# Performance work log

Hardware: AMD Instinct MI355X
Metric: run time of the kernel (lower is better)

Reference implementation:

```python
import jax, jax.numpy as jnp
import numpy as np

D_MODEL = 512
NUM_HEADS = 8
D_K = D_MODEL // NUM_HEADS
DIM_FF = 2048
EPS = 1e-5


def layer_norm(x, gamma, beta):
    mu = jnp.mean(x, axis=-1, keepdims=True)
    var = jnp.mean(jnp.square(x - mu), axis=-1, keepdims=True)
    return (x - mu) * jax.lax.rsqrt(var + EPS) * gamma + beta


def setup_inputs() -> dict:
    key = jax.random.key(0)
    ks = jax.random.split(key, 10)
    B, L = 8, 1024
    s = 1.0 / np.sqrt(D_MODEL)
    return {
        "h": jax.random.normal(ks[0], (B, L, D_MODEL), jnp.float32),
        "attn_bias": jax.random.normal(ks[1], (B, NUM_HEADS, L, L), jnp.float32),
        "mask": jnp.ones((B, L), jnp.int32),
        "Wqkv": jax.random.normal(ks[2], (D_MODEL, 3 * D_MODEL), jnp.float32) * s,
        "bqkv": jnp.zeros((3 * D_MODEL,), jnp.float32),
        "Wo": jax.random.normal(ks[3], (D_MODEL, D_MODEL), jnp.float32) * s,
        "bo": jnp.zeros((D_MODEL,), jnp.float32),
        "W1": jax.random.normal(ks[4], (D_MODEL, DIM_FF), jnp.float32) * s,
        "b1": jnp.zeros((DIM_FF,), jnp.float32),
        "W2": jax.random.normal(ks[5], (DIM_FF, D_MODEL), jnp.float32) * (1.0 / np.sqrt(DIM_FF)),
        "b2": jnp.zeros((D_MODEL,), jnp.float32),
        "g1": jnp.ones((D_MODEL,), jnp.float32),
        "be1": jnp.zeros((D_MODEL,), jnp.float32),
        "g2": jnp.ones((D_MODEL,), jnp.float32),
        "be2": jnp.zeros((D_MODEL,), jnp.float32),
    }


def reference(h, attn_bias, mask, Wqkv, bqkv, Wo, bo, W1, b1, W2, b2, g1, be1, g2, be2):
    B, L, D = h.shape
    H, dk = NUM_HEADS, D_K
    qkv = h @ Wqkv + bqkv                      # [B, L, 3D]
    q, k, v = jnp.split(qkv, 3, axis=-1)
    q = q.reshape(B, L, H, dk).transpose(0, 2, 1, 3)  # [B, H, L, dk]
    k = k.reshape(B, L, H, dk).transpose(0, 2, 1, 3)
    v = v.reshape(B, L, H, dk).transpose(0, 2, 1, 3)
    scores = jnp.einsum('bhqd,bhkd->bhqk', q, k) / np.sqrt(dk)
    scores = scores + attn_bias
    scores = jnp.where(mask[:, None, None, :] > 0, scores, -jnp.inf)
    attn = jax.nn.softmax(scores, axis=-1)
    out = jnp.einsum('bhqk,bhkd->bhqd', attn, v)       # [B, H, L, dk]
    out = out.transpose(0, 2, 1, 3).reshape(B, L, D)
    out = out @ Wo + bo
    h = layer_norm(h + out, g1, be1)
    ff = jax.nn.relu(h @ W1 + b1) @ W2 + b2
    h = layer_norm(h + ff, g2, be2)
    return h
```

## Files before the change

kernel.cpp:

```cpp
#include <hip/hip_runtime.h>
#include <hip/hip_bf16.h>
#include <math.h>

#define NUM_HEADS 8
#define SEQ_L 1024
#define EPS 1e-5f
#define KVBLK 64

typedef __bf16 bf16x8 __attribute__((ext_vector_type(8)));
typedef float f32x4 __attribute__((ext_vector_type(4)));
typedef __hip_bfloat16 bf16;

#define AS1 __attribute__((address_space(1)))
#define AS3 __attribute__((address_space(3)))

__device__ __forceinline__ void gload_lds16(const void* g, void* l) {
    __builtin_amdgcn_global_load_lds((const AS1 unsigned*)g, (AS3 unsigned*)l, 16, 0, 0);
}

__device__ __forceinline__ unsigned short bfb(float x) {
    bf16 b = __float2bfloat16(x);
    return *(unsigned short*)&b;
}

__device__ __forceinline__ int swz64(int el, int row) { return el ^ ((row & 7) << 3); }

__global__ __launch_bounds__(256) void f32_to_bf16_kernel(
    const float* __restrict__ in, bf16* __restrict__ out, int n)
{
    const int i = (blockIdx.x * 256 + threadIdx.x) * 4;
    if (i >= n) return;
    const float4 v = *(const float4*)&in[i];
    out[i + 0] = __float2bfloat16(v.x);
    out[i + 1] = __float2bfloat16(v.y);
    out[i + 2] = __float2bfloat16(v.z);
    out[i + 3] = __float2bfloat16(v.w);
}

__global__ __launch_bounds__(256) void transpose_w(
    const float* __restrict__ W, bf16* __restrict__ Wt, int K, int N)
{
    __shared__ float t[32][33];
    const int tx = threadIdx.x & 31, ty = threadIdx.x >> 5;
    const int n0 = blockIdx.x * 32, k0 = blockIdx.y * 32;
    #pragma unroll
    for (int r = 0; r < 4; ++r)
        t[ty + 8 * r][tx] = W[(size_t)(k0 + ty + 8 * r) * N + n0 + tx];
    __syncthreads();
    #pragma unroll
    for (int r = 0; r < 4; ++r)
        Wt[(size_t)(n0 + ty + 8 * r) * K + k0 + tx] = __float2bfloat16(t[tx][ty + 8 * r]);
}

__global__ __launch_bounds__(256) void gemm_bf16(
    const bf16* __restrict__ A, const bf16* __restrict__ Bt,
    const float* __restrict__ bias,
    float* __restrict__ C, bf16* __restrict__ Cb,
    int M, int N, int K, int relu)
{
    __shared__ __align__(16) bf16 Abuf[128 * 32];
    __shared__ __align__(16) bf16 Bbuf[128 * 32];
    const int tid = threadIdx.x;
    const int wv = tid >> 6, lane = tid & 63;
    const int row0 = blockIdx.y * 128, col0 = blockIdx.x * 128;
    const int wm = (wv >> 1) * 64, wn = (wv & 1) * 64;
    const int r0 = lane & 15, kb = lane >> 4;

    f32x4 acc[4][4] = {};
    const int arow = lane >> 2;
    const int akoff = (lane & 3) * 8;

    for (int k0 = 0; k0 < K; k0 += 32) {
        #pragma unroll
        for (int s = 0; s < 2; ++s) {
            const int c = 2 * wv + s;
            gload_lds16(&A[(size_t)(row0 + c * 16 + arow) * K + k0 + akoff], &Abuf[c * 512]);
            gload_lds16(&Bt[(size_t)(col0 + c * 16 + arow) * K + k0 + akoff], &Bbuf[c * 512]);
        }
        __syncthreads();

        bf16x8 a[4], b[4];
        #pragma unroll
        for (int i = 0; i < 4; ++i)
            a[i] = *(const bf16x8*)&Abuf[(wm + i * 16 + r0) * 32 + kb * 8];
        #pragma unroll
        for (int j = 0; j < 4; ++j)
            b[j] = *(const bf16x8*)&Bbuf[(wn + j * 16 + r0) * 32 + kb * 8];
        #pragma unroll
        for (int i = 0; i < 4; ++i)
            #pragma unroll
            for (int j = 0; j < 4; ++j)
                acc[i][j] = __builtin_amdgcn_mfma_f32_16x16x32_bf16(a[i], b[j], acc[i][j], 0, 0, 0);
        __syncthreads();
    }

    float bv[4];
    #pragma unroll
    for (int j = 0; j < 4; ++j) bv[j] = bias[col0 + wn + j * 16 + r0];

    #pragma unroll
    for (int i = 0; i < 4; ++i) {
        #pragma unroll
        for (int j = 0; j < 4; ++j) {
            const int col = col0 + wn + j * 16 + r0;
            #pragma unroll
            for (int reg = 0; reg < 4; ++reg) {
                const int row = row0 + wm + i * 16 + kb * 4 + reg;
                float v = acc[i][j][reg] + bv[j];
                if (relu) v = fmaxf(v, 0.f);
                if (C)  C[(size_t)row * N + col] = v;
                if (Cb) Cb[(size_t)row * N + col] = __float2bfloat16(v);
            }
        }
    }
}

__global__ __launch_bounds__(256) void gemm_qkv(
    const bf16* __restrict__ A, const bf16* __restrict__ Bt,
    const float* __restrict__ bias,
    bf16* __restrict__ Qb, bf16* __restrict__ Kb, bf16* __restrict__ Vtb,
    int M, int N, int K)
{
    __shared__ __align__(16) bf16 Abuf[128 * 32];
    __shared__ __align__(16) bf16 Bbuf[128 * 32];
    const int tid = threadIdx.x;
    const int wv = tid >> 6, lane = tid & 63;
    const int row0 = blockIdx.y * 128, col0 = blockIdx.x * 128;
    const int wm = (wv >> 1) * 64, wn = (wv & 1) * 64;
    const int r0 = lane & 15, kb = lane >> 4;

    f32x4 acc[4][4] = {};
    const int arow = lane >> 2;
    const int akoff = (lane & 3) * 8;

    for (int k0 = 0; k0 < K; k0 += 32) {
        #pragma unroll
        for (int s = 0; s < 2; ++s) {
            const int c = 2 * wv + s;
            gload_lds16(&A[(size_t)(row0 + c * 16 + arow) * K + k0 + akoff], &Abuf[c * 512]);
            gload_lds16(&Bt[(size_t)(col0 + c * 16 + arow) * K + k0 + akoff], &Bbuf[c * 512]);
        }
        __syncthreads();

        bf16x8 a[4], b[4];
        #pragma unroll
        for (int i = 0; i < 4; ++i)
            a[i] = *(const bf16x8*)&Abuf[(wm + i * 16 + r0) * 32 + kb * 8];
        #pragma unroll
        for (int j = 0; j < 4; ++j)
            b[j] = *(const bf16x8*)&Bbuf[(wn + j * 16 + r0) * 32 + kb * 8];
        #pragma unroll
        for (int i = 0; i < 4; ++i)
            #pragma unroll
            for (int j = 0; j < 4; ++j)
                acc[i][j] = __builtin_amdgcn_mfma_f32_16x16x32_bf16(a[i], b[j], acc[i][j], 0, 0, 0);
        __syncthreads();
    }

    #pragma unroll
    for (int i = 0; i < 4; ++i) {
        #pragma unroll
        for (int j = 0; j < 4; ++j) {
            const int col = col0 + wn + j * 16 + r0;
            const float bv = bias[col];
            const int region = col >> 9;
            const int cc = col & 511;
            const int head = cc >> 6, d = cc & 63;
            const int l0 = row0 + wm + i * 16 + kb * 4;
            const int b_ = l0 >> 10, l_ = l0 & 1023;
            if (region == 2) {
                unsigned short pk[4];
                #pragma unroll
                for (int reg = 0; reg < 4; ++reg) pk[reg] = bfb(acc[i][j][reg] + bv);
                *(ushort4*)&Vtb[((size_t)(b_ * NUM_HEADS + head) * 64 + d) * SEQ_L + l_] =
                    make_ushort4(pk[0], pk[1], pk[2], pk[3]);
            } else {
                const float s = (region == 0) ? 0.125f : 1.0f;
                bf16* dst = (region == 0) ? Qb : Kb;
                #pragma unroll
                for (int reg = 0; reg < 4; ++reg) {
                    dst[((size_t)(b_ * NUM_HEADS + head) * SEQ_L + l_ + reg) * 64 + d] =
                        __float2bfloat16((acc[i][j][reg] + bv) * s);
                }
            }
        }
    }
}

__global__ __launch_bounds__(256) void attn_mfma(
    const bf16* __restrict__ Qb, const bf16* __restrict__ Kb,
    const bf16* __restrict__ Vtb, const float* __restrict__ abias,
    const int* __restrict__ mask, bf16* __restrict__ out)
{
    const int bh = blockIdx.y;
    const int b = bh >> 3, h = bh & 7;
    const int q0 = blockIdx.x * 64;
    const int tid = threadIdx.x;
    const int wv = tid >> 6, lane = tid & 63;
    const int ql = lane & 15;
    const int hi = lane >> 4;

    __shared__ __align__(16) bf16 Ks[KVBLK * 64];
    __shared__ __align__(16) bf16 Vs[64 * KVBLK];
    __shared__ __align__(16) bf16 Ps[4][16 * 64];
    __shared__ float maskf[KVBLK];

    const int qrow = q0 + wv * 16 + ql;
    bf16x8 qf[2];
    #pragma unroll
    for (int kk = 0; kk < 2; ++kk)
        qf[kk] = *(const bf16x8*)&Qb[((size_t)bh * SEQ_L + qrow) * 64 + kk * 32 + hi * 8];

    f32x4 o[4] = {};
    float m = -1e30f, l = 0.f;

    const size_t bias_row = ((size_t)(b * NUM_HEADS + h) * SEQ_L + qrow) * SEQ_L;

    for (int k0 = 0; k0 < SEQ_L; k0 += KVBLK) {
        __syncthreads();
        {
            const int r = tid >> 3;
            const int c8 = (tid & 7) * 8;
            #pragma unroll
            for (int it = 0; it < 2; ++it) {
                const int row = r + it * 32;
                bf16x8 kv = *(const bf16x8*)&Kb[((size_t)bh * SEQ_L + k0 + row) * 64 + c8];
                *(bf16x8*)&Ks[swz64(row * 64 + c8, row)] = kv;
                bf16x8 vv = *(const bf16x8*)&Vtb[((size_t)bh * 64 + row) * SEQ_L + k0 + c8];
                *(bf16x8*)&Vs[swz64(row * 64 + c8, row)] = vv;
            }
            if (tid < KVBLK)
                maskf[tid] = (mask[b * SEQ_L + k0 + tid] > 0) ? 0.f : -1e30f;
        }
        __syncthreads();

        f32x4 bias4[4];
        #pragma unroll
        for (int c = 0; c < 4; ++c)
            bias4[c] = *(const f32x4*)&abias[bias_row + k0 + c * 16 + hi * 4];

        float p[4][4];
        #pragma unroll
        for (int c = 0; c < 4; ++c) {
            f32x4 sacc = {};
            #pragma unroll
            for (int kk = 0; kk < 2; ++kk) {
                const int row = c * 16 + ql;
                bf16x8 kf = *(const bf16x8*)&Ks[swz64(row * 64 + kk * 32 + hi * 8, row)];
                sacc = __builtin_amdgcn_mfma_f32_16x16x32_bf16(kf, qf[kk], sacc, 0, 0, 0);
            }
            const f32x4 mk = *(const f32x4*)&maskf[c * 16 + hi * 4];
            #pragma unroll
            for (int reg = 0; reg < 4; ++reg)
                p[c][reg] = sacc[reg] + bias4[c][reg] + mk[reg];
        }

        float mx = p[0][0];
        #pragma unroll
        for (int c = 0; c < 4; ++c)
            #pragma unroll
            for (int reg = 0; reg < 4; ++reg) mx = fmaxf(mx, p[c][reg]);
        mx = fmaxf(mx, __shfl_xor(mx, 16, 64));
        mx = fmaxf(mx, __shfl_xor(mx, 32, 64));

        const float mnew = fmaxf(m, mx);
        const float scale = __expf(m - mnew);
        m = mnew;
        float lsum = 0.f;
        #pragma unroll
        for (int c = 0; c < 4; ++c)
            #pragma unroll
            for (int reg = 0; reg < 4; ++reg) {
                const float pv = (p[c][reg] > -1e29f) ? __expf(p[c][reg] - mnew) : 0.f;
                p[c][reg] = pv;
                lsum += pv;
            }
        lsum += __shfl_xor(lsum, 16, 64);
        lsum += __shfl_xor(lsum, 32, 64);
        l = l * scale + lsum;

        #pragma unroll
        for (int c = 0; c < 4; ++c)
            #pragma unroll
            for (int s2 = 0; s2 < 2; ++s2) {
                const int el = ql * 64 + c * 16 + hi * 4 + 2 * s2;
                const unsigned pk = (unsigned)bfb(p[c][2 * s2]) |
                                    ((unsigned)bfb(p[c][2 * s2 + 1]) << 16);
                *(unsigned*)&Ps[wv][swz64(el, ql)] = pk;
            }

        #pragma unroll
        for (int reg = 0; reg < 4; ++reg) {
            const float sc_q = __shfl(scale, (lane & 48) | (hi * 4 + reg), 64);
            #pragma unroll
            for (int c2 = 0; c2 < 4; ++c2) o[c2][reg] *= sc_q;
        }

        #pragma unroll
        for (int kk = 0; kk < 2; ++kk) {
            bf16x8 pf = *(const bf16x8*)&Ps[wv][swz64(ql * 64 + kk * 32 + hi * 8, ql)];
            #pragma unroll
            for (int c2 = 0; c2 < 4; ++c2) {
                const int vrow = c2 * 16 + ql;
                bf16x8 vf = *(const bf16x8*)&Vs[swz64(vrow * 64 + kk * 32 + hi * 8, vrow)];
                o[c2] = __builtin_amdgcn_mfma_f32_16x16x32_bf16(pf, vf, o[c2], 0, 0, 0);
            }
        }
    }

    const float invl = (l > 0.f) ? (1.0f / l) : 0.f;
    #pragma unroll
    for (int reg = 0; reg < 4; ++reg) {
        const float inv_q = __shfl(invl, (lane & 48) | (hi * 4 + reg), 64);
        const int row = q0 + wv * 16 + hi * 4 + reg;
        #pragma unroll
        for (int c2 = 0; c2 < 4; ++c2)
            out[((size_t)(b * SEQ_L + row)) * 512 + h * 64 + c2 * 16 + ql] =
                __float2bfloat16(o[c2][reg] * inv_q);
    }
}

__global__ __launch_bounds__(256) void add_ln_kernel(
    const float* __restrict__ X, const float* __restrict__ Y,
    const float* __restrict__ gamma, const float* __restrict__ beta,
    float* __restrict__ out, bf16* __restrict__ outb)
{
    const int wave = threadIdx.x >> 6;
    const int lane = threadIdx.x & 63;
    const int row = blockIdx.x * 4 + wave;
    const float* xp = X + (size_t)row * 512 + lane * 8;
    const float* yp = Y + (size_t)row * 512 + lane * 8;

    float v[8];
    const float4 a0 = *(const float4*)xp;
    const float4 a1 = *(const float4*)(xp + 4);
    const float4 b0 = *(const float4*)yp;
    const float4 b1 = *(const float4*)(yp + 4);
    v[0] = a0.x + b0.x; v[1] = a0.y + b0.y; v[2] = a0.z + b0.z; v[3] = a0.w + b0.w;
    v[4] = a1.x + b1.x; v[5] = a1.y + b1.y; v[6] = a1.z + b1.z; v[7] = a1.w + b1.w;

    float s = 0.f, sq = 0.f;
    #pragma unroll
    for (int i = 0; i < 8; ++i) { s += v[i]; sq += v[i] * v[i]; }
    #pragma unroll
    for (int off = 1; off < 64; off <<= 1) {
        s += __shfl_xor(s, off, 64);
        sq += __shfl_xor(sq, off, 64);
    }
    const float mu = s * (1.f / 512.f);
    const float var = sq * (1.f / 512.f) - mu * mu;
    const float rstd = rsqrtf(var + EPS);

    const int c = lane * 8;
    const float4 g0 = *(const float4*)&gamma[c];
    const float4 g1 = *(const float4*)&gamma[c + 4];
    const float4 e0 = *(const float4*)&beta[c];
    const float4 e1 = *(const float4*)&beta[c + 4];
    float r[8];
    r[0] = (v[0] - mu) * rstd * g0.x + e0.x;
    r[1] = (v[1] - mu) * rstd * g0.y + e0.y;
    r[2] = (v[2] - mu) * rstd * g0.z + e0.z;
    r[3] = (v[3] - mu) * rstd * g0.w + e0.w;
    r[4] = (v[4] - mu) * rstd * g1.x + e1.x;
    r[5] = (v[5] - mu) * rstd * g1.y + e1.y;
    r[6] = (v[6] - mu) * rstd * g1.z + e1.z;
    r[7] = (v[7] - mu) * rstd * g1.w + e1.w;

    float* op = out + (size_t)row * 512 + c;
    *(float4*)op = make_float4(r[0], r[1], r[2], r[3]);
    *(float4*)(op + 4) = make_float4(r[4], r[5], r[6], r[7]);
    if (outb) {
        bf16* ob = outb + (size_t)row * 512 + c;
        #pragma unroll
        for (int i = 0; i < 8; ++i) ob[i] = __float2bfloat16(r[i]);
    }
}

extern "C" void kernel_launch(void* const* d_in, const int* in_sizes, int n_in,
                              void* d_out, int out_size, void* d_ws, size_t ws_size,
                              hipStream_t stream)
{
    const float* h    = (const float*)d_in[0];
    const float* ab   = (const float*)d_in[1];
    const int*   mask = (const int*)d_in[2];
    const float* Wqkv = (const float*)d_in[3];
    const float* bqkv = (const float*)d_in[4];
    const float* Wo   = (const float*)d_in[5];
    const float* bo   = (const float*)d_in[6];
    const float* W1   = (const float*)d_in[7];
    const float* b1   = (const float*)d_in[8];
    const float* W2   = (const float*)d_in[9];
    const float* b2   = (const float*)d_in[10];
    const float* g1   = (const float*)d_in[11];
    const float* be1  = (const float*)d_in[12];
    const float* g2   = (const float*)d_in[13];
    const float* be2  = (const float*)d_in[14];
    float* out = (float*)d_out;
    char* ws = (char*)d_ws;

    const int M = 8 * 1024;
    const size_t MB = 1024 * 1024;

    bf16*  hb   = (bf16*)(ws + 0 * MB);
    bf16*  Wtq  = (bf16*)(ws + 8 * MB);
    bf16*  Wto  = (bf16*)(ws + 10 * MB);
    bf16*  Wt1  = (bf16*)(ws + 11 * MB);
    bf16*  Wt2  = (bf16*)(ws + 13 * MB);
    bf16*  Qb   = (bf16*)(ws + 15 * MB);
    bf16*  Kb   = (bf16*)(ws + 23 * MB);
    bf16*  Vtb  = (bf16*)(ws + 31 * MB);
    bf16*  aob  = (bf16*)(ws + 39 * MB);
    float* proj = (float*)(ws + 47 * MB);
    float* h1   = (float*)(ws + 63 * MB);
    bf16*  h1b  = (bf16*)(ws + 79 * MB);
    bf16*  ffb  = (bf16*)(ws + 15 * MB);
    float* f2   = (float*)(ws + 47 * MB);

    f32_to_bf16_kernel<<<dim3(M * 512 / 1024), 256, 0, stream>>>(h, hb, M * 512);
    transpose_w<<<dim3(1536 / 32, 512 / 32), 256, 0, stream>>>(Wqkv, Wtq, 512, 1536);
    transpose_w<<<dim3(512 / 32, 512 / 32), 256, 0, stream>>>(Wo, Wto, 512, 512);
    transpose_w<<<dim3(2048 / 32, 512 / 32), 256, 0, stream>>>(W1, Wt1, 512, 2048);
    transpose_w<<<dim3(512 / 32, 2048 / 32), 256, 0, stream>>>(W2, Wt2, 2048, 512);

    gemm_qkv<<<dim3(1536 / 128, M / 128), 256, 0, stream>>>(hb, Wtq, bqkv, Qb, Kb, Vtb, M, 1536, 512);
    attn_mfma<<<dim3(SEQ_L / 64, 64), 256, 0, stream>>>(Qb, Kb, Vtb, ab, mask, aob);
    gemm_bf16<<<dim3(512 / 128, M / 128), 256, 0, stream>>>(aob, Wto, bo, proj, nullptr, M, 512, 512, 0);
    add_ln_kernel<<<dim3(M / 4), 256, 0, stream>>>(h, proj, g1, be1, h1, h1b);
    gemm_bf16<<<dim3(2048 / 128, M / 128), 256, 0, stream>>>(h1b, Wt1, b1, nullptr, ffb, M, 2048, 512, 1);
    gemm_bf16<<<dim3(512 / 128, M / 128), 256, 0, stream>>>(ffb, Wt2, b2, f2, nullptr, M, 512, 2048, 0);
    add_ln_kernel<<<dim3(M / 4), 256, 0, stream>>>(h1, f2, g2, be2, out, nullptr);
}
```

Before: 268.3 us.

## Double-buffer K/V tiles with register prefetch and use exp2 softmax in attention

```diff
diff --git a/kernel.cpp b/kernel.cpp
--- a/kernel.cpp
+++ b/kernel.cpp
@@ -6,6 +6,7 @@
 #define SEQ_L 1024
 #define EPS 1e-5f
 #define KVBLK 64
+#define LOG2E 1.44269504088896f
 
 typedef __bf16 bf16x8 __attribute__((ext_vector_type(8)));
 typedef float f32x4 __attribute__((ext_vector_type(4)));
@@ -175,7 +176,7 @@
                 *(ushort4*)&Vtb[((size_t)(b_ * NUM_HEADS + head) * 64 + d) * SEQ_L + l_] =
                     make_ushort4(pk[0], pk[1], pk[2], pk[3]);
             } else {
-                const float s = (region == 0) ? 0.125f : 1.0f;
+                const float s = (region == 0) ? (0.125f * LOG2E) : 1.0f;
                 bf16* dst = (region == 0) ? Qb : Kb;
                 #pragma unroll
                 for (int reg = 0; reg < 4; ++reg) {
@@ -200,10 +201,10 @@
     const int ql = lane & 15;
     const int hi = lane >> 4;
 
-    __shared__ __align__(16) bf16 Ks[KVBLK * 64];
-    __shared__ __align__(16) bf16 Vs[64 * KVBLK];
+    __shared__ __align__(16) bf16 Ks[2][KVBLK * 64];
+    __shared__ __align__(16) bf16 Vs[2][64 * KVBLK];
     __shared__ __align__(16) bf16 Ps[4][16 * 64];
-    __shared__ float maskf[KVBLK];
+    __shared__ float maskf[2][KVBLK];
 
     const int qrow = q0 + wv * 16 + ql;
     bf16x8 qf[2];
@@ -211,49 +212,73 @@
     for (int kk = 0; kk < 2; ++kk)
         qf[kk] = *(const bf16x8*)&Qb[((size_t)bh * SEQ_L + qrow) * 64 + kk * 32 + hi * 8];
 
+    const int sr = tid >> 3;
+    const int sc8 = (tid & 7) * 8;
+
     f32x4 o[4] = {};
     float m = -1e30f, l = 0.f;
-
     const size_t bias_row = ((size_t)(b * NUM_HEADS + h) * SEQ_L + qrow) * SEQ_L;
 
+    bf16x8 kreg[2], vreg[2];
+    f32x4 bias_raw[4];
+    float mreg = 0.f;
+    #pragma unroll
+    for (int it = 0; it < 2; ++it) {
+        const int row = sr + it * 32;
+        kreg[it] = *(const bf16x8*)&Kb[((size_t)bh * SEQ_L + row) * 64 + sc8];
+        vreg[it] = *(const bf16x8*)&Vtb[((size_t)bh * 64 + row) * SEQ_L + sc8];
+    }
+    #pragma unroll
+    for (int c = 0; c < 4; ++c)
+        bias_raw[c] = *(const f32x4*)&abias[bias_row + c * 16 + hi * 4];
+    if (tid < KVBLK) mreg = (mask[b * SEQ_L + tid] > 0) ? 0.f : -1e30f;
+    #pragma unroll
+    for (int it = 0; it < 2; ++it) {
+        const int row = sr + it * 32;
+        *(bf16x8*)&Ks[0][swz64(row * 64 + sc8, row)] = kreg[it];
+        *(bf16x8*)&Vs[0][swz64(row * 64 + sc8, row)] = vreg[it];
+    }
+    if (tid < KVBLK) maskf[0][tid] = mreg;
+
+    int cur = 0;
     for (int k0 = 0; k0 < SEQ_L; k0 += KVBLK) {
+        const bool more = (k0 + KVBLK) < SEQ_L;
+        f32x4 biasn[4];
+        if (more) {
+            const int k1 = k0 + KVBLK;
+            #pragma unroll
+            for (int it = 0; it < 2; ++it) {
+                const int row = sr + it * 32;
+                kreg[it] = *(const bf16x8*)&Kb[((size_t)bh * SEQ_L + k1 + row) * 64 + sc8];
+                vreg[it] = *(const bf16x8*)&Vtb[((size_t)bh * 64 + row) * SEQ_L + k1 + sc8];
+            }
+            #pragma unroll
+            for (int c = 0; c < 4; ++c)
+                biasn[c] = *(const f32x4*)&abias[bias_row + k1 + c * 16 + hi * 4];
+            if (tid < KVBLK) mreg = (mask[b * SEQ_L + k1 + tid] > 0) ? 0.f : -1e30f;
+        }
         __syncthreads();
-        {
-            const int r = tid >> 3;
-            const int c8 = (tid & 7) * 8;
-            #pragma unroll
-            for (int it = 0; it < 2; ++it) {
-                const int row = r + it * 32;
-                bf16x8 kv = *(const bf16x8*)&Kb[((size_t)bh * SEQ_L + k0 + row) * 64 + c8];
-                *(bf16x8*)&Ks[swz64(row * 64 + c8, row)] = kv;
-                bf16x8 vv = *(const bf16x8*)&Vtb[((size_t)bh * 64 + row) * SEQ_L + k0 + c8];
-                *(bf16x8*)&Vs[swz64(row * 64 + c8, row)] = vv;
-            }
-            if (tid < KVBLK)
-                maskf[tid] = (mask[b * SEQ_L + k0 + tid] > 0) ? 0.f : -1e30f;
-        }
-        __syncthreads();
-
-        f32x4 bias4[4];
-        #pragma unroll
-        for (int c = 0; c < 4; ++c)
-            bias4[c] = *(const f32x4*)&abias[bias_row + k0 + c * 16 + hi * 4];
-
-        float p[4][4];
+
+        f32x4 p[4];
         #pragma unroll
         for (int c = 0; c < 4; ++c) {
-            f32x4 sacc = {};
+            const f32x4 mk = *(const f32x4*)&maskf[cur][c * 16 + hi * 4];
+            #pragma unroll
+            for (int reg = 0; reg < 4; ++reg)
+                p[c][reg] = fmaf(bias_raw[c][reg], LOG2E, mk[reg]);
+        }
+
+        __builtin_amdgcn_s_setprio(1);
+        #pragma unroll
+        for (int c = 0; c < 4; ++c) {
+            const int row = c * 16 + ql;
             #pragma unroll
             for (int kk = 0; kk < 2; ++kk) {
-                const int row = c * 16 + ql;
-                bf16x8 kf = *(const bf16x8*)&Ks[swz64(row * 64 + kk * 32 + hi * 8, row)];
-                sacc = __builtin_amdgcn_mfma_f32_16x16x32_bf16(kf, qf[kk], sacc, 0, 0, 0);
-            }
-            const f32x4 mk = *(const f32x4*)&maskf[c * 16 + hi * 4];
-            #pragma unroll
-            for (int reg = 0; reg < 4; ++reg)
-                p[c][reg] = sacc[reg] + bias4[c][reg] + mk[reg];
-        }
+                bf16x8 kf = *(const bf16x8*)&Ks[cur][swz64(row * 64 + kk * 32 + hi * 8, row)];
+                p[c] = __builtin_amdgcn_mfma_f32_16x16x32_bf16(kf, qf[kk], p[c], 0, 0, 0);
+            }
+        }
+        __builtin_amdgcn_s_setprio(0);
 
         float mx = p[0][0];
         #pragma unroll
@@ -264,14 +289,14 @@
         mx = fmaxf(mx, __shfl_xor(mx, 32, 64));
 
         const float mnew = fmaxf(m, mx);
-        const float scale = __expf(m - mnew);
+        const float scale = __builtin_exp2f(m - mnew);
         m = mnew;
         float lsum = 0.f;
         #pragma unroll
         for (int c = 0; c < 4; ++c)
             #pragma unroll
             for (int reg = 0; reg < 4; ++reg) {
-                const float pv = (p[c][reg] > -1e29f) ? __expf(p[c][reg] - mnew) : 0.f;
+                const float pv = __builtin_exp2f(p[c][reg] - mnew);
                 p[c][reg] = pv;
                 lsum += pv;
             }
@@ -280,14 +305,13 @@
         l = l * scale + lsum;
 
         #pragma unroll
-        for (int c = 0; c < 4; ++c)
-            #pragma unroll
-            for (int s2 = 0; s2 < 2; ++s2) {
-                const int el = ql * 64 + c * 16 + hi * 4 + 2 * s2;
-                const unsigned pk = (unsigned)bfb(p[c][2 * s2]) |
-                                    ((unsigned)bfb(p[c][2 * s2 + 1]) << 16);
-                *(unsigned*)&Ps[wv][swz64(el, ql)] = pk;
-            }
+        for (int c = 0; c < 4; ++c) {
+            const int el = ql * 64 + c * 16 + hi * 4;
+            uint2 pk;
+            pk.x = (unsigned)bfb(p[c][0]) | ((unsigned)bfb(p[c][1]) << 16);
+            pk.y = (unsigned)bfb(p[c][2]) | ((unsigned)bfb(p[c][3]) << 16);
+            *(uint2*)&Ps[wv][swz64(el, ql)] = pk;
+        }
 
         #pragma unroll
         for (int reg = 0; reg < 4; ++reg) {
@@ -296,16 +320,31 @@
             for (int c2 = 0; c2 < 4; ++c2) o[c2][reg] *= sc_q;
         }
 
+        __builtin_amdgcn_s_setprio(1);
         #pragma unroll
         for (int kk = 0; kk < 2; ++kk) {
             bf16x8 pf = *(const bf16x8*)&Ps[wv][swz64(ql * 64 + kk * 32 + hi * 8, ql)];
             #pragma unroll
             for (int c2 = 0; c2 < 4; ++c2) {
                 const int vrow = c2 * 16 + ql;
-                bf16x8 vf = *(const bf16x8*)&Vs[swz64(vrow * 64 + kk * 32 + hi * 8, vrow)];
+                bf16x8 vf = *(const bf16x8*)&Vs[cur][swz64(vrow * 64 + kk * 32 + hi * 8, vrow)];
                 o[c2] = __builtin_amdgcn_mfma_f32_16x16x32_bf16(pf, vf, o[c2], 0, 0, 0);
             }
         }
+        __builtin_amdgcn_s_setprio(0);
+
+        if (more) {
+            #pragma unroll
+            for (int it = 0; it < 2; ++it) {
+                const int row = sr + it * 32;
+                *(bf16x8*)&Ks[cur ^ 1][swz64(row * 64 + sc8, row)] = kreg[it];
+                *(bf16x8*)&Vs[cur ^ 1][swz64(row * 64 + sc8, row)] = vreg[it];
+            }
+            if (tid < KVBLK) maskf[cur ^ 1][tid] = mreg;
+            #pragma unroll
+            for (int c = 0; c < 4; ++c) bias_raw[c] = biasn[c];
+        }
+        cur ^= 1;
     }
 
     const float invl = (l > 0.f) ? (1.0f / l) : 0.f;
```

Result: slower. 277.1 us (+3.3%).
